# Performance work log

Measured on AMD Instinct MI355X. Metric: run time of the kernel, lower is better.

The kernel has to match this reference:

```python
import itertools
import jax, jax.numpy as jnp
import numpy as np

LATENT_DIM = 8
N = 2 * LATENT_DIM  # width of z_combined = concat([z, dz])
BATCH = 131072

# Static combinatorial index sets, matching the nested-loop order
# (i <= j [<= k]) of the torch implementation exactly.
_PAIRS = np.array(list(itertools.combinations_with_replacement(range(N), 2)), dtype=np.int32)   # [136, 2]
_TRIPLES = np.array(list(itertools.combinations_with_replacement(range(N), 3)), dtype=np.int32)  # [816, 3]


def setup_inputs() -> dict:
    key = jax.random.key(0)
    k1, k2 = jax.random.split(key)
    z = jax.random.normal(k1, (BATCH, LATENT_DIM), dtype=jnp.float32)
    dz = jax.random.normal(k2, (BATCH, LATENT_DIM), dtype=jnp.float32)
    return {"z": z, "dz": dz}


def reference(z, dz):
    # z, dz: [B, latent_dim] -> Theta: [B, 985]
    zc = jnp.concatenate([z, dz], axis=1)  # [B, N]
    B = zc.shape[0]
    ones = jnp.ones((B, 1), dtype=zc.dtype)
    # degree-2 terms: zc[:, i] * zc[:, j] for i <= j, all at once via gather
    deg2 = zc[:, _PAIRS[:, 0]] * zc[:, _PAIRS[:, 1]]  # [B, 136]
    # degree-3 terms: zc[:, i] * zc[:, j] * zc[:, k] for i <= j <= k
    deg3 = zc[:, _TRIPLES[:, 0]] * zc[:, _TRIPLES[:, 1]] * zc[:, _TRIPLES[:, 2]]  # [B, 816]
    sine = jnp.sin(zc)  # [B, N]
    return jnp.concatenate([ones, zc, deg2, deg3, sine], axis=1)  # [B, 985]
```

## Files before the change

kernel.cpp:

```cpp
#include <hip/hip_runtime.h>
#include <cstddef>

#define NCOLS 985
#define TROWS 4
#define TILEF (TROWS * NCOLS)
#define NU    (TILEF / 4)
#define GSTR  176

__global__ __launch_bounds__(256) void sindy_kernel(const float* __restrict__ z,
                                                    const float* __restrict__ dz,
                                                    float* __restrict__ out, int batch,
                                                    int ntiles) {
  __shared__ unsigned int ctab[1024];
  __shared__ unsigned short ptab[136];
  __shared__ float G4[4][GSTR];
  __shared__ alignas(16) float buf[2][TILEF];

  const int tid = threadIdx.x;

  for (int c = tid; c < 1024; c += 256) {
    unsigned goff, midx;
    if (c < 153)      { goff = (unsigned)c; midx = 0; }
    else if (c < 969) {
      int t = c - 153, i = 0;
      for (;;) { int cnt = (16 - i) * (17 - i) / 2; if (t < cnt) break; t -= cnt; ++i; }
      goff = (unsigned)(17 + (136 - (16 - i) * (17 - i) / 2) + t);
      midx = (unsigned)(1 + i);
    }
    else if (c < 985) { goff = (unsigned)(153 + (c - 969)); midx = 0; }
    else              { goff = 169; midx = 169; }
    ctab[c] = goff | (midx << 16);
  }
  for (int e = tid; e < 136; e += 256) {
    int p = e, i = 0; while (p >= 16 - i) { p -= 16 - i; ++i; }
    ptab[e] = (unsigned short)(i | ((i + p) << 4));
  }
  __syncthreads();

  const int w = tid >> 6, l = tid & 63;

  unsigned ct[16];
  #pragma unroll
  for (int s = 0; s < 16; ++s) ct[s] = ctab[s * 64 + l];
  const unsigned pe0 = ptab[l];
  const unsigned pe1 = ptab[64 + l];
  const unsigned pe2 = ptab[(128 + l < 136) ? (128 + l) : 135];

  float* Gw = G4[w];

  auto compute_row = [&](int row, float* rb) {
    float gval = 0.f;
    if (l == 0)       gval = 1.0f;
    else if (l < 9)   gval = z [(size_t)row * 8 + (l - 1)];
    else if (l < 17)  gval = dz[(size_t)row * 8 + (l - 9)];
    const int gaddr = (l < 17) ? l : (152 + l);
    if (l < 24) Gw[gaddr] = gval;

    const float sv = __shfl(gval, l + 1);
    if (l < 16) Gw[153 + l] = __sinf(sv);
    __builtin_amdgcn_sched_barrier(0);

    {
      float a0 = Gw[1 + (pe0 & 15)], b0 = Gw[1 + (pe0 >> 4)];
      Gw[17 + l] = a0 * b0;
      float a1 = Gw[1 + (pe1 & 15)], b1 = Gw[1 + (pe1 >> 4)];
      Gw[17 + 64 + l] = a1 * b1;
      if (l < 8) {
        float a2 = Gw[1 + (pe2 & 15)], b2 = Gw[1 + (pe2 >> 4)];
        Gw[17 + 128 + l] = a2 * b2;
      }
    }
    __builtin_amdgcn_sched_barrier(0);

    #pragma unroll
    for (int s = 0; s < 16; ++s) {
      const unsigned e = ct[s];
      const float v = Gw[e & 0xffffu] * Gw[e >> 16];
      if (s < 15)      rb[s * 64 + l] = v;
      else if (l < 25) rb[960 + l] = v;
    }
  };

  auto drain_tile = [&](const float* src, float4* __restrict__ dst, int nelem) {
    if (nelem == TILEF) {
      const float4* s4 = (const float4*)src;
      #pragma unroll
      for (int k = 0; k < 4; ++k) {
        const int u = k * 256 + tid;
        if (k < 3 || u < NU) dst[u] = s4[u];
      }
    } else {
      float* __restrict__ d = (float*)dst;
      for (int u = tid; u < nelem; u += 256) d[u] = src[u];
    }
  };

  int t = blockIdx.x;
  if (t >= ntiles) return;
  int p = 0;
  {
    const int row = t * TROWS + w;
    if (row < batch) compute_row(row, buf[0] + w * NCOLS);
  }
  __syncthreads();

  for (int tn = t + gridDim.x; tn < ntiles; tn += gridDim.x) {
    const int nel = min(TILEF, batch * NCOLS - t * TILEF);
    drain_tile(buf[p], (float4*)(out + (size_t)t * TILEF), nel);
    {
      const int row = tn * TROWS + w;
      if (row < batch) compute_row(row, buf[p ^ 1] + w * NCOLS);
    }
    __syncthreads();
    p ^= 1; t = tn;
  }
  {
    const int nel = min(TILEF, batch * NCOLS - t * TILEF);
    drain_tile(buf[p], (float4*)(out + (size_t)t * TILEF), nel);
  }
}

extern "C" void kernel_launch(void* const* d_in, const int* in_sizes, int n_in,
                              void* d_out, int out_size, void* d_ws, size_t ws_size,
                              hipStream_t stream) {
  const float* z  = (const float*)d_in[0];
  const float* dz = (const float*)d_in[1];
  float* out = (float*)d_out;
  const int batch = in_sizes[0] / 8;

  const int ntiles = (batch + TROWS - 1) / TROWS;
  const int blocks = 2048;
  sindy_kernel<<<blocks, 256, 0, stream>>>(z, dz, out, batch, ntiles);
}
```

Before: 117.2 us.

## Vectorize tile compute with float4 shared-multiplier units and fuse drain into compute loop

Doubles rows per tile to 8 and precomputes a per-tile element table. Groups of four consecutive outputs that share one multiplier are classified as 'normal' and computed as float4 with a single multiplier load; the few straddling groups go through a scalar fallback list. The global-store drain of the previous tile is interleaved with computing the current tile inside one unrolled loop. The aim is to cut LDS gather traffic and overlap stores with compute, at the cost of roughly double the shared-memory footprint, which may reduce blocks per CU.

```diff
diff --git a/kernel.cpp b/kernel.cpp
--- a/kernel.cpp
+++ b/kernel.cpp
@@ -2,121 +2,179 @@
 #include <cstddef>
 
 #define NCOLS 985
-#define TROWS 4
+#define TROWS 8
 #define TILEF (TROWS * NCOLS)
-#define NU    (TILEF / 4)
+#define NUNIT (TILEF / 4)
 #define GSTR  176
+#define GTOT  (TROWS * GSTR)
+#define MAXSTR 192
 
 __global__ __launch_bounds__(256) void sindy_kernel(const float* __restrict__ z,
                                                     const float* __restrict__ dz,
                                                     float* __restrict__ out, int batch,
                                                     int ntiles) {
-  __shared__ unsigned int ctab[1024];
+  __shared__ alignas(16) float buf[2][TILEF];
+  __shared__ float Gsh[GTOT];
+  __shared__ alignas(16) unsigned int sel[MAXSTR * 4];
+  __shared__ unsigned short sdst[MAXSTR];
   __shared__ unsigned short ptab[136];
-  __shared__ float G4[4][GSTR];
-  __shared__ alignas(16) float buf[2][TILEF];
+  __shared__ int cnt[2];
 
   const int tid = threadIdx.x;
+  const int w = tid >> 6, l = tid & 63;
 
-  for (int c = tid; c < 1024; c += 256) {
+  unsigned int* etab  = (unsigned int*)buf[0];
+  uint2*        nlist = (uint2*)buf[1];
+
+  if (tid < 2) cnt[tid] = 0;
+  for (int e = tid; e < 136; e += 256) {
+    int p = e, i = 0; while (p >= 16 - i) { p -= 16 - i; ++i; }
+    ptab[e] = (unsigned short)(i | ((i + p) << 4));
+  }
+  for (int fe = tid; fe < TILEF; fe += 256) {
+    const int r = fe / NCOLS;
+    const int c = fe - r * NCOLS;
     unsigned goff, midx;
     if (c < 153)      { goff = (unsigned)c; midx = 0; }
     else if (c < 969) {
       int t = c - 153, i = 0;
-      for (;;) { int cnt = (16 - i) * (17 - i) / 2; if (t < cnt) break; t -= cnt; ++i; }
+      for (;;) { int cn = (16 - i) * (17 - i) / 2; if (t < cn) break; t -= cn; ++i; }
       goff = (unsigned)(17 + (136 - (16 - i) * (17 - i) / 2) + t);
       midx = (unsigned)(1 + i);
     }
-    else if (c < 985) { goff = (unsigned)(153 + (c - 969)); midx = 0; }
-    else              { goff = 169; midx = 169; }
-    ctab[c] = goff | (midx << 16);
-  }
-  for (int e = tid; e < 136; e += 256) {
-    int p = e, i = 0; while (p >= 16 - i) { p -= 16 - i; ++i; }
-    ptab[e] = (unsigned short)(i | ((i + p) << 4));
+    else              { goff = (unsigned)(153 + (c - 969)); midx = 0; }
+    const unsigned base = (unsigned)(r * GSTR);
+    etab[fe] = (base + goff) | ((base + midx) << 16);
   }
   __syncthreads();
 
-  const int w = tid >> 6, l = tid & 63;
+  for (int u = tid; u < NUNIT; u += 256) {
+    const unsigned e0 = etab[4 * u];
+    const unsigned g0 = e0 & 0xffffu, m = e0 >> 16;
+    const bool normal =
+      etab[4 * u + 1] == ((g0 + 1) | (m << 16)) &&
+      etab[4 * u + 2] == ((g0 + 2) | (m << 16)) &&
+      etab[4 * u + 3] == ((g0 + 3) | (m << 16));
+    if (normal) {
+      int s = atomicAdd(&cnt[0], 1);
+      nlist[s] = make_uint2((unsigned)u, e0);
+    } else {
+      int s = atomicAdd(&cnt[1], 1);
+      if (s < MAXSTR) {
+        sdst[s] = (unsigned short)u;
+        sel[4 * s + 0] = etab[4 * u + 0];
+        sel[4 * s + 1] = etab[4 * u + 1];
+        sel[4 * s + 2] = etab[4 * u + 2];
+        sel[4 * s + 3] = etab[4 * u + 3];
+      }
+    }
+  }
+  __syncthreads();
+  const int n_norm = cnt[0];
+  const int n_str  = cnt[1];
 
-  unsigned ct[16];
+  uint2 ne[8];
   #pragma unroll
-  for (int s = 0; s < 16; ++s) ct[s] = ctab[s * 64 + l];
+  for (int k = 0; k < 8; ++k) {
+    const int idx = k * 256 + tid;
+    ne[k] = (idx < n_norm) ? nlist[idx] : make_uint2(0u, 0u);
+  }
+  __syncthreads();
+
   const unsigned pe0 = ptab[l];
   const unsigned pe1 = ptab[64 + l];
   const unsigned pe2 = ptab[(128 + l < 136) ? (128 + l) : 135];
 
-  float* Gw = G4[w];
-
-  auto compute_row = [&](int row, float* rb) {
-    float gval = 0.f;
-    if (l == 0)       gval = 1.0f;
-    else if (l < 9)   gval = z [(size_t)row * 8 + (l - 1)];
-    else if (l < 17)  gval = dz[(size_t)row * 8 + (l - 9)];
-    const int gaddr = (l < 17) ? l : (152 + l);
-    if (l < 24) Gw[gaddr] = gval;
-
-    const float sv = __shfl(gval, l + 1);
-    if (l < 16) Gw[153 + l] = __sinf(sv);
-    __builtin_amdgcn_sched_barrier(0);
-
-    {
-      float a0 = Gw[1 + (pe0 & 15)], b0 = Gw[1 + (pe0 >> 4)];
-      Gw[17 + l] = a0 * b0;
-      float a1 = Gw[1 + (pe1 & 15)], b1 = Gw[1 + (pe1 >> 4)];
-      Gw[17 + 64 + l] = a1 * b1;
-      if (l < 8) {
-        float a2 = Gw[1 + (pe2 & 15)], b2 = Gw[1 + (pe2 >> 4)];
-        Gw[17 + 128 + l] = a2 * b2;
+  auto stage_rows = [&](int row0) {
+    #pragma unroll
+    for (int rr = 0; rr < 2; ++rr) {
+      const int lr  = 2 * w + rr;
+      const int row = row0 + lr;
+      float* Gr = Gsh + lr * GSTR;
+      if (row < batch) {
+        float gval = 0.f;
+        if (l == 0)       gval = 1.0f;
+        else if (l < 9)   gval = z [(size_t)row * 8 + (l - 1)];
+        else if (l < 17)  gval = dz[(size_t)row * 8 + (l - 9)];
+        const int gaddr = (l < 17) ? l : (152 + l);
+        if (l < 24) Gr[gaddr] = gval;
+        const float sv = __shfl(gval, l + 1);
+        if (l < 16) Gr[153 + l] = __sinf(sv);
+        __builtin_amdgcn_sched_barrier(0);
+        {
+          float a0 = Gr[1 + (pe0 & 15)], b0 = Gr[1 + (pe0 >> 4)];
+          Gr[17 + l] = a0 * b0;
+          float a1 = Gr[1 + (pe1 & 15)], b1 = Gr[1 + (pe1 >> 4)];
+          Gr[17 + 64 + l] = a1 * b1;
+          if (l < 8) {
+            float a2 = Gr[1 + (pe2 & 15)], b2 = Gr[1 + (pe2 >> 4)];
+            Gr[17 + 128 + l] = a2 * b2;
+          }
+        }
+        __builtin_amdgcn_sched_barrier(0);
       }
-    }
-    __builtin_amdgcn_sched_barrier(0);
-
-    #pragma unroll
-    for (int s = 0; s < 16; ++s) {
-      const unsigned e = ct[s];
-      const float v = Gw[e & 0xffffu] * Gw[e >> 16];
-      if (s < 15)      rb[s * 64 + l] = v;
-      else if (l < 25) rb[960 + l] = v;
-    }
-  };
-
-  auto drain_tile = [&](const float* src, float4* __restrict__ dst, int nelem) {
-    if (nelem == TILEF) {
-      const float4* s4 = (const float4*)src;
-      #pragma unroll
-      for (int k = 0; k < 4; ++k) {
-        const int u = k * 256 + tid;
-        if (k < 3 || u < NU) dst[u] = s4[u];
-      }
-    } else {
-      float* __restrict__ d = (float*)dst;
-      for (int u = tid; u < nelem; u += 256) d[u] = src[u];
     }
   };
 
   int t = blockIdx.x;
-  if (t >= ntiles) return;
   int p = 0;
-  {
-    const int row = t * TROWS + w;
-    if (row < batch) compute_row(row, buf[0] + w * NCOLS);
-  }
-  __syncthreads();
+  int t_prev = -1;
+  for (; t < ntiles; t += gridDim.x) {
+    stage_rows(t * TROWS);
+    __syncthreads();
 
-  for (int tn = t + gridDim.x; tn < ntiles; tn += gridDim.x) {
-    const int nel = min(TILEF, batch * NCOLS - t * TILEF);
-    drain_tile(buf[p], (float4*)(out + (size_t)t * TILEF), nel);
-    {
-      const int row = tn * TROWS + w;
-      if (row < batch) compute_row(row, buf[p ^ 1] + w * NCOLS);
+    float* bw = buf[p];
+    const float4* dsrc = (const float4*)buf[p ^ 1];
+    float4* __restrict__ dglob =
+        (t_prev >= 0) ? (float4*)(out + (size_t)t_prev * TILEF) : (float4*)out;
+
+    #pragma unroll
+    for (int k = 0; k < 8; ++k) {
+      if (t_prev >= 0) {
+        const int u = k * 256 + tid;
+        if (k < 7 || u < NUNIT) dglob[u] = dsrc[u];
+      }
+      {
+        const int idx = k * 256 + tid;
+        const unsigned uu = ne[k].x;
+        const unsigned g0 = ne[k].y & 0xffffu;
+        const unsigned m  = ne[k].y >> 16;
+        const float mv = Gsh[m];
+        const float a0 = Gsh[g0], a1 = Gsh[g0 + 1], a2 = Gsh[g0 + 2], a3 = Gsh[g0 + 3];
+        float4 v; v.x = a0 * mv; v.y = a1 * mv; v.z = a2 * mv; v.w = a3 * mv;
+        if (idx < n_norm) *(float4*)&bw[4 * uu] = v;
+      }
+    }
+    if (tid < n_str) {
+      const int uu = sdst[tid];
+      const unsigned e0 = sel[4 * tid], e1 = sel[4 * tid + 1];
+      const unsigned e2 = sel[4 * tid + 2], e3 = sel[4 * tid + 3];
+      float4 v;
+      v.x = Gsh[e0 & 0xffffu] * Gsh[e0 >> 16];
+      v.y = Gsh[e1 & 0xffffu] * Gsh[e1 >> 16];
+      v.z = Gsh[e2 & 0xffffu] * Gsh[e2 >> 16];
+      v.w = Gsh[e3 & 0xffffu] * Gsh[e3 >> 16];
+      *(float4*)&bw[4 * uu] = v;
     }
     __syncthreads();
-    p ^= 1; t = tn;
+    t_prev = t; p ^= 1;
   }
-  {
-    const int nel = min(TILEF, batch * NCOLS - t * TILEF);
-    drain_tile(buf[p], (float4*)(out + (size_t)t * TILEF), nel);
+
+  if (t_prev >= 0) {
+    const float4* dsrc = (const float4*)buf[p ^ 1];
+    const int nel = batch * NCOLS - t_prev * TILEF;
+    float4* __restrict__ dglob = (float4*)(out + (size_t)t_prev * TILEF);
+    if (nel >= TILEF) {
+      #pragma unroll
+      for (int k = 0; k < 8; ++k) {
+        const int u = k * 256 + tid;
+        if (k < 7 || u < NUNIT) dglob[u] = dsrc[u];
+      }
+    } else {
+      const float* s = (const float*)dsrc;
+      float* d = (float*)dglob;
+      for (int u = tid; u < nel; u += 256) d[u] = s[u];
+    }
   }
 }
 
```

Result: slower. 175.3 us (+49.6%).
